# Performance work log

Measured on AMD Instinct MI355X. Metric: run time of the kernel, lower is better.

## Reference

```python
import jax, jax.numpy as jnp
import numpy as np
from jax import lax

IMG_W = 1024.0
IMG_H = 1024.0
CONF_THRESH = 0.5
NMS_THRESH = 0.3
MAX_DELTA = 2.0
K_PRE = 300   # pre-NMS candidates per image per level
K_OUT = 10    # keep[:10] per image per level, as in the torch code


def _make_anchors(hw, stride, base, scales=(0.5, 1.0, 1.5), ars=(0.5, 1.0, 2.0)):
    # anchor index a is outermost to match permute(0,1,3,4,2).reshape ordering
    whs = np.array([[base * sc * np.sqrt(ar), base * sc / np.sqrt(ar)]
                    for sc in scales for ar in ars], dtype=np.float32)  # [A,2]
    c = (np.arange(hw, dtype=np.float32) + 0.5) * stride
    cy, cx = np.meshgrid(c, c, indexing='ij')
    cx = cx.reshape(-1)[None, :]  # [1,HW]
    cy = cy.reshape(-1)[None, :]
    w = whs[:, 0:1]
    h = whs[:, 1:2]
    anc = np.stack([cx - 0.5 * w, cy - 0.5 * h, cx + 0.5 * w, cy + 0.5 * h], axis=-1)  # [A,HW,4]
    return jnp.asarray(anc.reshape(-1, 4))


def setup_inputs() -> dict:
    key = jax.random.key(0)
    ks = jax.random.split(key, 8)
    B, A = 16, 9
    hws = [128, 64, 32, 16]
    strides = [8, 16, 32, 64]
    bases = [64, 128, 256, 512]
    inp = {}
    for li in range(4):
        inp[f'cls{li}'] = jax.random.normal(ks[li], (B, A, 1, hws[li], hws[li]), jnp.float32)
        inp[f'box{li}'] = 0.3 * jax.random.normal(ks[li + 4], (B, A, 4, hws[li], hws[li]), jnp.float32)
        inp[f'anc{li}'] = _make_anchors(hws[li], strides[li], bases[li])
    return inp


def decode_boxes(deltas, anchors):
    # deltas: [B,N,4], anchors: [1,N,4] (broadcast). Faithful to apply_deltas_to_anchors.
    w = anchors[..., 2] - anchors[..., 0]
    h = anchors[..., 3] - anchors[..., 1]
    cx = anchors[..., 0] + 0.5 * w
    cy = anchors[..., 1] + 0.5 * h
    d = jnp.clip(deltas, -MAX_DELTA, MAX_DELTA)
    px = cx + d[..., 0] * w
    py = cy + d[..., 1] * h
    pw = w * jnp.exp(d[..., 2])
    ph = h * jnp.exp(d[..., 3])
    x1 = jnp.clip(px - 0.5 * pw, 0.0, IMG_W)
    y1 = jnp.clip(py - 0.5 * ph, 0.0, IMG_H)
    x2 = jnp.clip(px + 0.5 * pw, 0.0, IMG_W)
    y2 = jnp.clip(py + 0.5 * ph, 0.0, IMG_H)
    boxes = jnp.stack([x1, y1, x2, y2], axis=-1)
    bw = x2 - x1
    bh = y2 - y1
    valid = (bw > 1.0) & (bh > 1.0) & (bw < 2000.0) & (bh < 2000.0)
    return boxes, valid


def _pairwise_iou(b):
    # b: [K,4]
    area = (b[:, 2] - b[:, 0]) * (b[:, 3] - b[:, 1])
    x1 = jnp.maximum(b[:, None, 0], b[None, :, 0])
    y1 = jnp.maximum(b[:, None, 1], b[None, :, 1])
    x2 = jnp.minimum(b[:, None, 2], b[None, :, 2])
    y2 = jnp.minimum(b[:, None, 3], b[None, :, 3])
    inter = jnp.clip(x2 - x1, 0.0) * jnp.clip(y2 - y1, 0.0)
    return inter / (area[:, None] + area[None, :] - inter + 1e-9)


def _nms_image(boxes, masked_scores):
    # boxes: [N,4]; masked_scores: [N] (score if conf&valid else -1)
    topv, topi = lax.top_k(masked_scores, K_PRE)   # score-descending, like torchvision nms order
    b = boxes[topi]                                 # [K,4]
    ious = _pairwise_iou(b)
    idxs = jnp.arange(K_PRE)
    keep0 = topv > 0.0  # only candidates above conf thresh (>0.5) survive the mask fill of -1

    def body(i, keep):
        sup = (ious[i] > NMS_THRESH) & (idxs > i)
        return jnp.where(keep[i], keep & ~sup, keep)

    keep = lax.fori_loop(0, K_PRE, body, keep0)
    rank = jnp.cumsum(keep.astype(jnp.int32)) - 1
    sel = keep & (rank < K_OUT)                     # keep[:10]
    idx = jnp.where(sel, rank, K_OUT)               # dump slot K_OUT
    out_b = jnp.zeros((K_OUT + 1, 4), boxes.dtype).at[idx].set(b)[:K_OUT]
    out_s = jnp.zeros((K_OUT + 1,), topv.dtype).at[idx].set(topv)[:K_OUT]
    out_v = jnp.zeros((K_OUT + 1,), bool).at[idx].set(sel)[:K_OUT]
    return out_b, out_s, out_v


def _process_level(cls, box, anc):
    B = cls.shape[0]
    # [B,A,C,H,W] -> [B,A,H,W,C] -> [B,N]; C=1
    scores = jax.nn.sigmoid(jnp.transpose(cls, (0, 1, 3, 4, 2)).reshape(B, -1))
    deltas = jnp.transpose(box, (0, 1, 3, 4, 2)).reshape(B, -1, 4)
    pboxes, valid = decode_boxes(deltas, anc[None])
    masked = jnp.where((scores > CONF_THRESH) & valid, scores, -1.0)
    return jax.vmap(_nms_image)(pboxes, masked)  # ([B,10,4],[B,10],[B,10])


def reference(cls0, cls1, cls2, cls3, box0, box1, box2, box3, anc0, anc1, anc2, anc3):
    levels = [(cls0, box0, anc0), (cls1, box1, anc1), (cls2, box2, anc2), (cls3, box3, anc3)]
    outs = [_process_level(c, b, a) for (c, b, a) in levels]
    boxes = jnp.concatenate([o[0] for o in outs], axis=1)   # [B, 40, 4]
    scores = jnp.concatenate([o[1] for o in outs], axis=1)  # [B, 40]
    valid = jnp.concatenate([o[2] for o in outs], axis=1)   # [B, 40] bool
    out5 = jnp.concatenate([boxes, scores[..., None]], axis=-1)  # [B, 40, 5]
    return out5, valid
```

## Files before the change

### kernel.cpp

```cpp
#include <hip/hip_runtime.h>
#include <stdint.h>

#define NLEV 4
#define BIMG 16
#define NPROB 64
#define NB 1024
#define CAP 6144
#define BUF 2048
#define FK 512
#define KPRE 300
#define KOUT 10
#define NTHREADS 256
#define CHUNK 2048
#define CPI 97

__device__ __align__(16) int g_hist[NPROB * NB];
__device__ int g_count[NPROB];
__device__ int g_cut[NPROB];
__device__ unsigned long long g_cand[NPROB * CAP];

struct Params {
    const float* cls[NLEV];
    const float* box[NLEV];
    const float* anc[NLEV];
};

__device__ __constant__ int c_tbin[4] = {256, 179, 77, 0};
__device__ __constant__ int c_sh[4] = {14, 12, 10, 8};

__device__ __forceinline__ int bin_of(float x) {
    int b = (int)(x * (NB / 8.0f));
    return b > (NB - 1) ? (NB - 1) : b;
}

__device__ __forceinline__ bool decode_c(float d0, float d1, float d2, float d3,
                                         float4 an, float out[4]) {
#pragma clang fp contract(off)
    float w = an.z - an.x;
    float h = an.w - an.y;
    float cx = an.x + 0.5f * w;
    float cy = an.y + 0.5f * h;
    d0 = fminf(fmaxf(d0, -2.0f), 2.0f);
    d1 = fminf(fmaxf(d1, -2.0f), 2.0f);
    d2 = fminf(fmaxf(d2, -2.0f), 2.0f);
    d3 = fminf(fmaxf(d3, -2.0f), 2.0f);
    float px = cx + d0 * w;
    float py = cy + d1 * h;
    float pw = w * expf(d2);
    float ph = h * expf(d3);
    float x1 = fminf(fmaxf(px - 0.5f * pw, 0.0f), 1024.0f);
    float y1 = fminf(fmaxf(py - 0.5f * ph, 0.0f), 1024.0f);
    float x2 = fminf(fmaxf(px + 0.5f * pw, 0.0f), 1024.0f);
    float y2 = fminf(fmaxf(py + 0.5f * ph, 0.0f), 1024.0f);
    out[0] = x1; out[1] = y1; out[2] = x2; out[3] = y2;
    float bw = x2 - x1;
    float bh = y2 - y1;
    return (bw > 1.0f) && (bh > 1.0f) && (bw < 2000.0f) && (bh < 2000.0f);
}

__device__ __forceinline__ bool decode_one(const float* boxbase, const float* ancbase,
                                           int b, int e, int sh, float out[4]) {
    int HW = 1 << sh;
    int a = e >> sh;
    int hw = e & (HW - 1);
    const float* dB = boxbase + ((size_t)(b * 9 + a) * 4) * (size_t)HW + hw;
    float d0 = dB[0];
    float d1 = dB[(size_t)HW];
    float d2 = dB[(size_t)2 * HW];
    float d3 = dB[(size_t)3 * HW];
    float4 an = *(const float4*)(ancbase + (size_t)4 * e);
    return decode_c(d0, d1, d2, d3, an, out);
}

__device__ __forceinline__ void map_block(int c, int& level, int& chunk) {
    if (c < 72)      { level = 0; chunk = c; }
    else if (c < 90) { level = 1; chunk = c - 72; }
    else if (c < 95) { level = 2; chunk = c - 90; }
    else             { level = 3; chunk = c - 95; }
}

__global__ void k_init() {
    int i = blockIdx.x * blockDim.x + threadIdx.x;
    if (i < NPROB * NB) g_hist[i] = 0;
    if (i < NPROB) g_count[i] = 0;
}

__global__ __launch_bounds__(NTHREADS) void k_scan(Params P) {
    __shared__ int lh[NB];
    __shared__ unsigned long long buf[BUF];
    __shared__ int s_cnt, s_base;
    for (int i = threadIdx.x; i < NB; i += NTHREADS) lh[i] = 0;
    if (threadIdx.x == 0) s_cnt = 0;
    __syncthreads();

    int img = blockIdx.x / CPI;
    int level, chunk;
    map_block(blockIdx.x % CPI, level, chunk);
    int sh = c_sh[level];
    int tbin = c_tbin[level];
    int N4 = (9 << sh) >> 2;
    int HW = 1 << sh;
    const float4* cls4 = (const float4*)(P.cls[level] + (size_t)img * (9 << sh));
    const float* boxp = P.box[level];
    const float* ancp = P.anc[level];
    int base4 = (chunk * CHUNK) >> 2;

    int i4a = base4 + threadIdx.x;
    int i4b = base4 + NTHREADS + threadIdx.x;
    bool va = i4a < N4, vb = i4b < N4;
    float4 xa, xb;
    if (va) xa = cls4[i4a];
    if (vb) xb = cls4[i4b];

#pragma unroll
    for (int g = 0; g < 2; g++) {
        bool vg = g ? vb : va;
        if (!vg) continue;
        float4 x = g ? xb : xa;
        int e0 = 4 * (g ? i4b : i4a);
        float xs[4] = {x.x, x.y, x.z, x.w};
        int bins[4];
        bool hit = false;
#pragma unroll
        for (int c = 0; c < 4; c++) {
            bins[c] = (xs[c] > 0.f) ? bin_of(xs[c]) : -1;
            hit |= (bins[c] >= tbin);
        }
        if (!hit) continue;
        int a = e0 >> sh;
        int hw = e0 & (HW - 1);
        const float* plane = boxp + ((size_t)((img * 9 + a) * 4)) * (size_t)HW + hw;
        float4 d0 = *(const float4*)(plane);
        float4 d1 = *(const float4*)(plane + HW);
        float4 d2 = *(const float4*)(plane + 2 * (size_t)HW);
        float4 d3 = *(const float4*)(plane + 3 * (size_t)HW);
        const float4* anc4 = (const float4*)ancp + e0;
        float s0[4] = {d0.x, d0.y, d0.z, d0.w};
        float s1[4] = {d1.x, d1.y, d1.z, d1.w};
        float s2[4] = {d2.x, d2.y, d2.z, d2.w};
        float s3[4] = {d3.x, d3.y, d3.z, d3.w};
#pragma unroll
        for (int c = 0; c < 4; c++) {
            if (bins[c] >= tbin) {
                float bo[4];
                if (decode_c(s0[c], s1[c], s2[c], s3[c], anc4[c], bo)) {
                    atomicAdd(&lh[bins[c]], 1);
                    float s = 1.0f / (1.0f + expf(-xs[c]));
                    int e = e0 + c;
                    unsigned long long key =
                        ((unsigned long long)__float_as_uint(s) << 32) |
                        ((unsigned long long)(0x3FFFFu - (unsigned)e) << 10) |
                        (unsigned long long)bins[c];
                    int pos = atomicAdd(&s_cnt, 1);
                    buf[pos] = key;
                }
            }
        }
    }
    __syncthreads();

    int p = (level << 4) | img;
    int cnt = s_cnt;
    if (threadIdx.x == 0) s_base = atomicAdd(&g_count[p], cnt);
    __syncthreads();
    int base = s_base;
    for (int i = threadIdx.x; i < cnt; i += NTHREADS) {
        int j = base + i;
        if (j < CAP) g_cand[(size_t)p * CAP + j] = buf[i];
    }
    for (int i = threadIdx.x; i < NB; i += NTHREADS) {
        int v = lh[i];
        if (v) atomicAdd(&g_hist[p * NB + i], v);
    }
}

__global__ __launch_bounds__(NTHREADS) void k_cutoff() {
    __shared__ int suf[NTHREADS + 1];
    int p = blockIdx.x, t = threadIdx.x;
    int4 hv = ((const int4*)(g_hist + p * NB))[t];
    suf[t] = hv.x + hv.y + hv.z + hv.w;
    if (t == 0) suf[NTHREADS] = 0;
    __syncthreads();
    for (int off = 1; off < NTHREADS; off <<= 1) {
        int v = (t + off < NTHREADS) ? suf[t + off] : 0;
        __syncthreads();
        suf[t] += v;
        __syncthreads();
    }
    int shi = suf[t + 1];
    int slo = suf[t];
    if (slo >= KPRE && shi < KPRE) {
        int h4[4] = {hv.x, hv.y, hv.z, hv.w};
        int cum = shi, c = 0;
        for (int j = 3; j >= 0; j--) {
            cum += h4[j];
            if (cum >= KPRE) { c = 4 * t + j; break; }
        }
        g_cut[p] = c;
    }
    if (t == 0 && suf[0] < KPRE) g_cut[p] = 0;
}

__global__ __launch_bounds__(NTHREADS) void k_nms(Params P, float* out) {
    __shared__ unsigned long long skey[FK];
    __shared__ float bx[FK * 4];
    __shared__ float area[FK];
    __shared__ int alive[FK];
    __shared__ unsigned long long s_red[NTHREADS / 64];
    __shared__ unsigned long long s_chosen;
    __shared__ int s_scnt, s_cidx, s_selc, s_sel[KOUT];

    int p = blockIdx.x;
    int level = p >> 4, img = p & 15;
    int sh = c_sh[level];
    int tid = threadIdx.x;

    int n = g_count[p];
    if (n > CAP) n = CAP;
    int cut = g_cut[p];
    if (tid == 0) { s_scnt = 0; s_selc = 0; }
    __syncthreads();

    for (int i = tid; i < n; i += NTHREADS) {
        unsigned long long key = g_cand[(size_t)p * CAP + i];
        if ((int)(key & 1023u) >= cut) {
            int pos = atomicAdd(&s_scnt, 1);
            if (pos < FK) skey[pos] = key;
        }
    }
    __syncthreads();
    int m = s_scnt;
    if (m > FK) m = FK;

    for (int i = tid; i < m; i += NTHREADS) {
        unsigned long long key = skey[i];
        int e = (int)(0x3FFFFu - (unsigned)((key >> 10) & 0x3FFFFu));
        float bo[4];
        decode_one(P.box[level], P.anc[level], img, e, sh, bo);
        bx[i * 4 + 0] = bo[0];
        bx[i * 4 + 1] = bo[1];
        bx[i * 4 + 2] = bo[2];
        bx[i * 4 + 3] = bo[3];
        {
#pragma clang fp contract(off)
            area[i] = (bo[2] - bo[0]) * (bo[3] - bo[1]);
        }
    }
    __syncthreads();

    for (int i = tid; i < m; i += NTHREADS) {
        unsigned long long k = skey[i];
        int r = 0;
        for (int j = 0; j < m; j++) r += (skey[j] > k);
        alive[i] = (r < KPRE) ? 1 : 0;
    }
    __syncthreads();

    for (int it = 0; it < KOUT; it++) {
        unsigned long long loc = 0;
        for (int i = tid; i < m; i += NTHREADS)
            if (alive[i]) { unsigned long long k = skey[i]; if (k > loc) loc = k; }
        for (int off = 32; off; off >>= 1) {
            unsigned long long o = __shfl_down(loc, off, 64);
            if (o > loc) loc = o;
        }
        if ((tid & 63) == 0) s_red[tid >> 6] = loc;
        __syncthreads();
        if (tid == 0) {
            unsigned long long mx = s_red[0];
            for (int w = 1; w < NTHREADS / 64; w++) if (s_red[w] > mx) mx = s_red[w];
            s_chosen = mx;
        }
        __syncthreads();
        unsigned long long ch = s_chosen;
        if (ch == 0ull) break;
        for (int i = tid; i < m; i += NTHREADS)
            if (alive[i] && skey[i] == ch) { s_cidx = i; alive[i] = 0; }
        __syncthreads();
        int c = s_cidx;
        if (tid == 0) s_sel[s_selc++] = c;
        float cx1 = bx[c * 4 + 0], cy1 = bx[c * 4 + 1];
        float cx2 = bx[c * 4 + 2], cy2 = bx[c * 4 + 3];
        float ca = area[c];
        for (int i = tid; i < m; i += NTHREADS) {
            if (alive[i]) {
#pragma clang fp contract(off)
                float ix1 = fmaxf(cx1, bx[i * 4 + 0]);
                float iy1 = fmaxf(cy1, bx[i * 4 + 1]);
                float ix2 = fminf(cx2, bx[i * 4 + 2]);
                float iy2 = fminf(cy2, bx[i * 4 + 3]);
                float iw = fmaxf(ix2 - ix1, 0.0f);
                float ih = fmaxf(iy2 - iy1, 0.0f);
                float inter = iw * ih;
                float denom = (ca + area[i]) - inter + 1e-9f;
                float iou = inter / denom;
                if (iou > 0.3f) alive[i] = 0;
            }
        }
        __syncthreads();
    }
    __syncthreads();

    if (tid < KOUT) {
        float o0 = 0.f, o1 = 0.f, o2 = 0.f, o3 = 0.f, o4 = 0.f, ov = 0.f;
        if (tid < s_selc) {
            int c = s_sel[tid];
            o0 = bx[c * 4 + 0];
            o1 = bx[c * 4 + 1];
            o2 = bx[c * 4 + 2];
            o3 = bx[c * 4 + 3];
            o4 = __uint_as_float((unsigned)(skey[c] >> 32));
            ov = 1.0f;
        }
        int q = level * KOUT + tid;
        float* o5 = out + (size_t)img * 200 + (size_t)q * 5;
        o5[0] = o0; o5[1] = o1; o5[2] = o2; o5[3] = o3; o5[4] = o4;
        out[3200 + img * 40 + q] = ov;
    }
}

extern "C" void kernel_launch(void* const* d_in, const int* in_sizes, int n_in,
                              void* d_out, int out_size, void* d_ws, size_t ws_size,
                              hipStream_t stream) {
    Params P;
    for (int l = 0; l < 4; l++) {
        P.cls[l] = (const float*)d_in[3 * l + 0];
        P.box[l] = (const float*)d_in[3 * l + 1];
        P.anc[l] = (const float*)d_in[3 * l + 2];
    }
    float* out = (float*)d_out;
    k_init<<<(NPROB * NB + 255) / 256, 256, 0, stream>>>();
    k_scan<<<BIMG * CPI, NTHREADS, 0, stream>>>(P);
    k_cutoff<<<NPROB, NTHREADS, 0, stream>>>();
    k_nms<<<NPROB, NTHREADS, 0, stream>>>(P, out);
}
```

Measured before the change: 159.5 us.

## Drop global histogram and atomics; build histogram and cutoff inside NMS kernel

Each scan block now writes its candidates to a private per-chunk slot with its own count, instead of using global atomics for the candidate append and the per-bin histogram. The NMS kernel gathers the per-chunk lists through a prefix sum, builds the score histogram in shared memory, and computes the cutoff itself. This removes the init and cutoff kernels (two fewer launches) and the global atomic traffic. In exchange the 64 NMS blocks do more serial gather work and use much more shared memory (48KB key buffer), which may lower occupancy.

```diff
diff --git a/kernel.cpp b/kernel.cpp
--- a/kernel.cpp
+++ b/kernel.cpp
@@ -5,19 +5,18 @@
 #define BIMG 16
 #define NPROB 64
 #define NB 1024
-#define CAP 6144
 #define BUF 2048
+#define CPI 97
+#define TCH (BIMG * CPI)
+#define SKN 6144
 #define FK 512
 #define KPRE 300
 #define KOUT 10
 #define NTHREADS 256
 #define CHUNK 2048
-#define CPI 97
-
-__device__ __align__(16) int g_hist[NPROB * NB];
-__device__ int g_count[NPROB];
-__device__ int g_cut[NPROB];
-__device__ unsigned long long g_cand[NPROB * CAP];
+
+__device__ unsigned long long g_cand[TCH * BUF];
+__device__ int g_ccount[TCH];
 
 struct Params {
     const float* cls[NLEV];
@@ -26,7 +25,9 @@
 };
 
 __device__ __constant__ int c_tbin[4] = {256, 179, 77, 0};
-__device__ __constant__ int c_sh[4] = {14, 12, 10, 8};
+__device__ __constant__ int c_sh[4]   = {14, 12, 10, 8};
+__device__ __constant__ int c_cbase[4] = {0, 72, 90, 95};
+__device__ __constant__ int c_nch[4]   = {72, 18, 5, 2};
 
 __device__ __forceinline__ int bin_of(float x) {
     int b = (int)(x * (NB / 8.0f));
@@ -79,17 +80,9 @@
     else             { level = 3; chunk = c - 95; }
 }
 
-__global__ void k_init() {
-    int i = blockIdx.x * blockDim.x + threadIdx.x;
-    if (i < NPROB * NB) g_hist[i] = 0;
-    if (i < NPROB) g_count[i] = 0;
-}
-
 __global__ __launch_bounds__(NTHREADS) void k_scan(Params P) {
-    __shared__ int lh[NB];
     __shared__ unsigned long long buf[BUF];
-    __shared__ int s_cnt, s_base;
-    for (int i = threadIdx.x; i < NB; i += NTHREADS) lh[i] = 0;
+    __shared__ int s_cnt;
     if (threadIdx.x == 0) s_cnt = 0;
     __syncthreads();
 
@@ -144,7 +137,6 @@
             if (bins[c] >= tbin) {
                 float bo[4];
                 if (decode_c(s0[c], s1[c], s2[c], s3[c], anc4[c], bo)) {
-                    atomicAdd(&lh[bins[c]], 1);
                     float s = 1.0f / (1.0f + expf(-xs[c]));
                     int e = e0 + c;
                     unsigned long long key =
@@ -159,73 +151,90 @@
     }
     __syncthreads();
 
-    int p = (level << 4) | img;
     int cnt = s_cnt;
-    if (threadIdx.x == 0) s_base = atomicAdd(&g_count[p], cnt);
-    __syncthreads();
-    int base = s_base;
-    for (int i = threadIdx.x; i < cnt; i += NTHREADS) {
-        int j = base + i;
-        if (j < CAP) g_cand[(size_t)p * CAP + j] = buf[i];
-    }
-    for (int i = threadIdx.x; i < NB; i += NTHREADS) {
-        int v = lh[i];
-        if (v) atomicAdd(&g_hist[p * NB + i], v);
-    }
-}
-
-__global__ __launch_bounds__(NTHREADS) void k_cutoff() {
+    if (threadIdx.x == 0) g_ccount[blockIdx.x] = cnt;
+    unsigned long long* dst = g_cand + (size_t)blockIdx.x * BUF;
+    for (int i = threadIdx.x; i < cnt; i += NTHREADS) dst[i] = buf[i];
+}
+
+__global__ __launch_bounds__(NTHREADS) void k_nms(Params P, float* out) {
+    __shared__ unsigned long long skey[SKN];
+    __shared__ __align__(16) int lh[NB];
     __shared__ int suf[NTHREADS + 1];
-    int p = blockIdx.x, t = threadIdx.x;
-    int4 hv = ((const int4*)(g_hist + p * NB))[t];
-    suf[t] = hv.x + hv.y + hv.z + hv.w;
-    if (t == 0) suf[NTHREADS] = 0;
-    __syncthreads();
-    for (int off = 1; off < NTHREADS; off <<= 1) {
-        int v = (t + off < NTHREADS) ? suf[t + off] : 0;
-        __syncthreads();
-        suf[t] += v;
-        __syncthreads();
-    }
-    int shi = suf[t + 1];
-    int slo = suf[t];
-    if (slo >= KPRE && shi < KPRE) {
-        int h4[4] = {hv.x, hv.y, hv.z, hv.w};
-        int cum = shi, c = 0;
-        for (int j = 3; j >= 0; j--) {
-            cum += h4[j];
-            if (cum >= KPRE) { c = 4 * t + j; break; }
-        }
-        g_cut[p] = c;
-    }
-    if (t == 0 && suf[0] < KPRE) g_cut[p] = 0;
-}
-
-__global__ __launch_bounds__(NTHREADS) void k_nms(Params P, float* out) {
-    __shared__ unsigned long long skey[FK];
+    __shared__ int pre[80];
+    __shared__ unsigned long long surv[FK];
     __shared__ float bx[FK * 4];
     __shared__ float area[FK];
     __shared__ int alive[FK];
     __shared__ unsigned long long s_red[NTHREADS / 64];
     __shared__ unsigned long long s_chosen;
-    __shared__ int s_scnt, s_cidx, s_selc, s_sel[KOUT];
+    __shared__ int s_cut, s_scnt, s_cidx, s_selc, s_sel[KOUT];
 
     int p = blockIdx.x;
     int level = p >> 4, img = p & 15;
     int sh = c_sh[level];
     int tid = threadIdx.x;
-
-    int n = g_count[p];
-    if (n > CAP) n = CAP;
-    int cut = g_cut[p];
-    if (tid == 0) { s_scnt = 0; s_selc = 0; }
-    __syncthreads();
+    int nch = c_nch[level];
+    int gbase = img * CPI + c_cbase[level];
+
+    for (int i = tid; i < NB; i += NTHREADS) lh[i] = 0;
+    if (tid == 0) {
+        int acc = 0;
+        for (int c = 0; c < nch; c++) {
+            pre[c] = acc;
+            acc += g_ccount[gbase + c];
+        }
+        pre[nch] = acc > SKN ? SKN : acc;
+        s_scnt = 0;
+        s_selc = 0;
+    }
+    __syncthreads();
+    int n = pre[nch];
+
+    for (int j = tid; j < n; j += NTHREADS) {
+        int lo = 0, hi = nch - 1;
+        while (lo < hi) {
+            int mid = (lo + hi + 1) >> 1;
+            if (pre[mid] <= j) lo = mid; else hi = mid - 1;
+        }
+        unsigned long long key = g_cand[(size_t)(gbase + lo) * BUF + (j - pre[lo])];
+        skey[j] = key;
+        atomicAdd(&lh[(int)(key & 1023u)], 1);
+    }
+    __syncthreads();
+
+    {
+        int4 hv = ((const int4*)lh)[tid];
+        suf[tid] = hv.x + hv.y + hv.z + hv.w;
+        if (tid == 0) suf[NTHREADS] = 0;
+        __syncthreads();
+        for (int off = 1; off < NTHREADS; off <<= 1) {
+            int v = (tid + off < NTHREADS) ? suf[tid + off] : 0;
+            __syncthreads();
+            suf[tid] += v;
+            __syncthreads();
+        }
+        int shi = suf[tid + 1];
+        int slo = suf[tid];
+        if (slo >= KPRE && shi < KPRE) {
+            int h4[4] = {hv.x, hv.y, hv.z, hv.w};
+            int cum = shi, c = 0;
+            for (int j = 3; j >= 0; j--) {
+                cum += h4[j];
+                if (cum >= KPRE) { c = 4 * tid + j; break; }
+            }
+            s_cut = c;
+        }
+        if (tid == 0 && suf[0] < KPRE) s_cut = 0;
+    }
+    __syncthreads();
+    int cut = s_cut;
 
     for (int i = tid; i < n; i += NTHREADS) {
-        unsigned long long key = g_cand[(size_t)p * CAP + i];
+        unsigned long long key = skey[i];
         if ((int)(key & 1023u) >= cut) {
             int pos = atomicAdd(&s_scnt, 1);
-            if (pos < FK) skey[pos] = key;
+            if (pos < FK) surv[pos] = key;
         }
     }
     __syncthreads();
@@ -233,7 +242,7 @@
     if (m > FK) m = FK;
 
     for (int i = tid; i < m; i += NTHREADS) {
-        unsigned long long key = skey[i];
+        unsigned long long key = surv[i];
         int e = (int)(0x3FFFFu - (unsigned)((key >> 10) & 0x3FFFFu));
         float bo[4];
         decode_one(P.box[level], P.anc[level], img, e, sh, bo);
@@ -249,9 +258,9 @@
     __syncthreads();
 
     for (int i = tid; i < m; i += NTHREADS) {
-        unsigned long long k = skey[i];
+        unsigned long long k = surv[i];
         int r = 0;
-        for (int j = 0; j < m; j++) r += (skey[j] > k);
+        for (int j = 0; j < m; j++) r += (surv[j] > k);
         alive[i] = (r < KPRE) ? 1 : 0;
     }
     __syncthreads();
@@ -259,7 +268,7 @@
     for (int it = 0; it < KOUT; it++) {
         unsigned long long loc = 0;
         for (int i = tid; i < m; i += NTHREADS)
-            if (alive[i]) { unsigned long long k = skey[i]; if (k > loc) loc = k; }
+            if (alive[i]) { unsigned long long k = surv[i]; if (k > loc) loc = k; }
         for (int off = 32; off; off >>= 1) {
             unsigned long long o = __shfl_down(loc, off, 64);
             if (o > loc) loc = o;
@@ -275,7 +284,7 @@
         unsigned long long ch = s_chosen;
         if (ch == 0ull) break;
         for (int i = tid; i < m; i += NTHREADS)
-            if (alive[i] && skey[i] == ch) { s_cidx = i; alive[i] = 0; }
+            if (alive[i] && surv[i] == ch) { s_cidx = i; alive[i] = 0; }
         __syncthreads();
         int c = s_cidx;
         if (tid == 0) s_sel[s_selc++] = c;
@@ -309,7 +318,7 @@
             o1 = bx[c * 4 + 1];
             o2 = bx[c * 4 + 2];
             o3 = bx[c * 4 + 3];
-            o4 = __uint_as_float((unsigned)(skey[c] >> 32));
+            o4 = __uint_as_float((unsigned)(surv[c] >> 32));
             ov = 1.0f;
         }
         int q = level * KOUT + tid;
@@ -329,8 +338,6 @@
         P.anc[l] = (const float*)d_in[3 * l + 2];
     }
     float* out = (float*)d_out;
-    k_init<<<(NPROB * NB + 255) / 256, 256, 0, stream>>>();
-    k_scan<<<BIMG * CPI, NTHREADS, 0, stream>>>(P);
-    k_cutoff<<<NPROB, NTHREADS, 0, stream>>>();
+    k_scan<<<TCH, NTHREADS, 0, stream>>>(P);
     k_nms<<<NPROB, NTHREADS, 0, stream>>>(P, out);
 }
```

After: 157.3 us. About the same (-1.4%).
